# Performance work log

Measured on AMD Instinct MI355X. Metric: run time of the kernel, lower is better.

## Reference

```python
import jax, jax.numpy as jnp
import numpy as np

HEADS = 8
DIM_HEAD = 64
SCALE = DIM_HEAD ** (-0.5)


def _flatten_like_module(t):
    # Reproduces: jnp.transpose(t, (0,2,1,3)).reshape(t.shape[0], t.shape[1], t.shape[2]*t.shape[3])
    # where the reshape dims come from the ORIGINAL (pre-transpose) shape.
    B, S, H, Dh = t.shape
    return jnp.transpose(t, (0, 2, 1, 3)).reshape(B, S, H * Dh)


def _heads_to_batch(t):
    b, s, d = t.shape
    t = t.reshape(b, s, HEADS, d // HEADS)
    t = jnp.transpose(t, (0, 2, 1, 3))
    return t.reshape(b * HEADS, s, d // HEADS)


def setup_inputs() -> dict:
    key = jax.random.key(0)
    kq, kk, kv = jax.random.split(key, 3)
    shape = (2, 16384, 8, 64)  # [B, S, heads, dim_head]
    return {
        "query": jax.random.normal(kq, shape, dtype=jnp.float32),
        "key": jax.random.normal(kk, shape, dtype=jnp.float32),
        "value": jax.random.normal(kv, shape, dtype=jnp.float32),
    }


def reference(query, key, value):
    q = _heads_to_batch(_flatten_like_module(query))   # [B*H, S, Dh]
    k = _heads_to_batch(_flatten_like_module(key))     # [B*H, S, Dh]
    # Swapped contraction: reduce over the sequence axis -> [B*H, Dh, Dh]
    scores = jnp.einsum('bdi,bdj->bij', q, k) * SCALE
    probs = jax.nn.softmax(scores, axis=2)
    v = _heads_to_batch(_flatten_like_module(value))   # [B*H, S, Dh]
    # NOTE: computed in the original module but never returned (dead under jit DCE)
    _hidden = jnp.einsum('bij,bdj->bid', probs, v)     # [B*H, Dh, S]
    return probs
```

## Files before the change

### kernel.cpp

```cpp
#include <hip/hip_runtime.h>

#define NS 16384
#define BUCKETS 16

__device__ __forceinline__ void gload_lds16(const float* g, float* l) {
    __builtin_amdgcn_global_load_lds(
        (const __attribute__((address_space(1))) void*)g,
        (__attribute__((address_space(3))) void*)l,
        16 , 0, 0);
}

__global__ __launch_bounds__(256) void gram_partial(
    const float* __restrict__ Q, const float* __restrict__ K,
    float* __restrict__ part, int bpb, int shi_per_blk)
{
    const int bid    = blockIdx.x;
    const int bucket = bid / bpb;
    const int chunk  = bid % bpb;
    const int b      = bucket >> 3;
    const int r      = bucket & 7;

    const int tid  = threadIdx.x;
    const int lane = tid & 63;
    const int wv   = tid >> 6;
    const int ty   = tid >> 4;
    const int tx   = tid & 15;

    __shared__ __align__(16) float sbuf[2][4096];

    const float* gq = Q + (size_t)b * ((size_t)NS * 512)
                        + ((size_t)wv * 8 + r) * 512 + lane * 4;
    const float* gk = K + (size_t)b * ((size_t)NS * 512)
                        + ((size_t)wv * 8 + r) * 512 + lane * 4;
    const size_t base_off = (size_t)chunk * shi_per_blk * 4096;

    const int niter = shi_per_blk >> 2;

    auto stage = [&](int it, int bufi) {
        const size_t off = base_off + (size_t)it * 16384;
        float* dq = &sbuf[bufi][wv * 512];
        float* dk = &sbuf[bufi][2048 + wv * 512];
        gload_lds16(gq + off, dq);
        gload_lds16(gq + off + 256, dq + 256);
        gload_lds16(gk + off, dk);
        gload_lds16(gk + off + 256, dk + 256);
    };

    float acc[4][4] = {};

    stage(0, 0);
    for (int it = 0; it < niter; ++it) {
        __syncthreads();
        if (it + 1 < niter) stage(it + 1, (it + 1) & 1);
        const float* bq = &sbuf[it & 1][0];
        const float* bk = &sbuf[it & 1][2048];
        #pragma unroll
        for (int tr = 0; tr < 32; ++tr) {
            const float4 qv = *(const float4*)(bq + tr * 64 + ty * 4);
            const float4 kv = *(const float4*)(bk + tr * 64 + tx * 4);
            const float qa[4] = {qv.x, qv.y, qv.z, qv.w};
            const float ka[4] = {kv.x, kv.y, kv.z, kv.w};
            #pragma unroll
            for (int ii = 0; ii < 4; ++ii)
                #pragma unroll
                for (int jj = 0; jj < 4; ++jj)
                    acc[ii][jj] += qa[ii] * ka[jj];
        }
    }

    float* p = part + (size_t)bid * 4096;
    #pragma unroll
    for (int ii = 0; ii < 4; ++ii) {
        float4 v = make_float4(acc[ii][0], acc[ii][1], acc[ii][2], acc[ii][3]);
        *(float4*)(p + (ty * 4 + ii) * 64 + tx * 4) = v;
    }
}

__global__ __launch_bounds__(256) void reduce_softmax(
    const float* __restrict__ part, float* __restrict__ out, int slices)
{
    const int g   = blockIdx.x >> 6;
    const int row = blockIdx.x & 63;
    const int c   = threadIdx.x & 63;
    const int sl  = threadIdx.x >> 6;

    const float* p = part + (size_t)(g * (slices * 4) + sl * slices) * 4096
                          + row * 64 + c;
    float s = 0.f;
    #pragma unroll 4
    for (int k = 0; k < slices; ++k) s += p[(size_t)k * 4096];

    __shared__ float red[4][64];
    red[sl][c] = s;
    __syncthreads();
    if (sl == 0) {
        float v = (red[0][c] + red[1][c]) + (red[2][c] + red[3][c]);
        v *= 0.125f;
        float m = v;
        #pragma unroll
        for (int o = 32; o; o >>= 1) m = fmaxf(m, __shfl_xor(m, o));
        const float e = __expf(v - m);
        float sum = e;
        #pragma unroll
        for (int o = 32; o; o >>= 1) sum += __shfl_xor(sum, o);
        out[(size_t)g * 4096 + row * 64 + c] = e / sum;
    }
}

extern "C" void kernel_launch(void* const* d_in, const int* in_sizes, int n_in,
                              void* d_out, int out_size, void* d_ws, size_t ws_size,
                              hipStream_t stream)
{
    const float* Q = (const float*)d_in[0];
    const float* K = (const float*)d_in[1];
    float* out  = (float*)d_out;
    float* part = (float*)d_ws;

    int bpb = 64;
    while ((size_t)BUCKETS * bpb * 4096 * sizeof(float) > ws_size && bpb > 4) bpb >>= 1;
    const int shi_per_blk = 2048 / bpb;

    gram_partial<<<dim3(BUCKETS * bpb), dim3(256), 0, stream>>>(Q, K, part, bpb, shi_per_blk);
    reduce_softmax<<<dim3(1024), dim3(256), 0, stream>>>(part, out, bpb / 4);
}
```

Before: 189.4 us.

## Replace LDS-staged gram accumulation with direct global loads per wave quadrant

Removes the double-buffered LDS staging (global_load_lds plus __syncthreads) and has each wave compute one 32x32 quadrant of the 64x64 Gram tile, loading float4 values straight from global memory. Launch bounds now request 4 blocks per CU, which should raise occupancy. The aim is to drop LDS traffic and barrier stalls. The cost is redundant global loads, since each Q/K element is now read by two waves and the accesses are strided, so the kernel leans on the L1/L2 caches.

```diff
diff --git a/kernel.cpp b/kernel.cpp
--- a/kernel.cpp
+++ b/kernel.cpp
@@ -3,16 +3,9 @@
 #define NS 16384
 #define BUCKETS 16
 
-__device__ __forceinline__ void gload_lds16(const float* g, float* l) {
-    __builtin_amdgcn_global_load_lds(
-        (const __attribute__((address_space(1))) void*)g,
-        (__attribute__((address_space(3))) void*)l,
-        16 , 0, 0);
-}
-
-__global__ __launch_bounds__(256) void gram_partial(
+__global__ __launch_bounds__(256, 4) void gram_partial(
     const float* __restrict__ Q, const float* __restrict__ K,
-    float* __restrict__ part, int bpb, int shi_per_blk)
+    float* __restrict__ part, int bpb, int spb)
 {
     const int bid    = blockIdx.x;
     const int bucket = bid / bpb;
@@ -20,44 +13,27 @@
     const int b      = bucket >> 3;
     const int r      = bucket & 7;
 
-    const int tid  = threadIdx.x;
-    const int lane = tid & 63;
-    const int wv   = tid >> 6;
-    const int ty   = tid >> 4;
-    const int tx   = tid & 15;
+    const int lane = threadIdx.x & 63;
+    const int wv   = threadIdx.x >> 6;
+    const int ty   = lane >> 3;
+    const int tx   = lane & 7;
+    const int qcol = (wv >> 1) * 32 + ty * 4;
+    const int kcol = (wv & 1) * 32 + tx * 4;
 
-    __shared__ __align__(16) float sbuf[2][4096];
-
-    const float* gq = Q + (size_t)b * ((size_t)NS * 512)
-                        + ((size_t)wv * 8 + r) * 512 + lane * 4;
-    const float* gk = K + (size_t)b * ((size_t)NS * 512)
-                        + ((size_t)wv * 8 + r) * 512 + lane * 4;
-    const size_t base_off = (size_t)chunk * shi_per_blk * 4096;
-
-    const int niter = shi_per_blk >> 2;
-
-    auto stage = [&](int it, int bufi) {
-        const size_t off = base_off + (size_t)it * 16384;
-        float* dq = &sbuf[bufi][wv * 512];
-        float* dk = &sbuf[bufi][2048 + wv * 512];
-        gload_lds16(gq + off, dq);
-        gload_lds16(gq + off + 256, dq + 256);
-        gload_lds16(gk + off, dk);
-        gload_lds16(gk + off + 256, dk + 256);
-    };
+    const size_t tb = (size_t)b * ((size_t)NS * 512) + (size_t)r * 512;
+    const float* qp = Q + tb + qcol;
+    const float* kp = K + tb + kcol;
 
     float acc[4][4] = {};
 
-    stage(0, 0);
-    for (int it = 0; it < niter; ++it) {
-        __syncthreads();
-        if (it + 1 < niter) stage(it + 1, (it + 1) & 1);
-        const float* bq = &sbuf[it & 1][0];
-        const float* bk = &sbuf[it & 1][2048];
+    const int s0 = chunk * spb;
+    for (int s = s0; s < s0 + spb; ++s) {
+        const float* qb = qp + (size_t)s * 4096;
+        const float* kb = kp + (size_t)s * 4096;
         #pragma unroll
-        for (int tr = 0; tr < 32; ++tr) {
-            const float4 qv = *(const float4*)(bq + tr * 64 + ty * 4);
-            const float4 kv = *(const float4*)(bk + tr * 64 + tx * 4);
+        for (int h = 0; h < 8; ++h) {
+            const float4 qv = *(const float4*)(qb + h * 64);
+            const float4 kv = *(const float4*)(kb + h * 64);
             const float qa[4] = {qv.x, qv.y, qv.z, qv.w};
             const float ka[4] = {kv.x, kv.y, kv.z, kv.w};
             #pragma unroll
@@ -68,7 +44,8 @@
         }
     }
 
-    float* p = part + (size_t)bid * 4096;
+    float* p = part + (size_t)bid * 4096
+             + (size_t)((wv >> 1) * 32) * 64 + (wv & 1) * 32;
     #pragma unroll
     for (int ii = 0; ii < 4; ++ii) {
         float4 v = make_float4(acc[ii][0], acc[ii][1], acc[ii][2], acc[ii][3]);
@@ -118,8 +95,8 @@
 
     int bpb = 64;
     while ((size_t)BUCKETS * bpb * 4096 * sizeof(float) > ws_size && bpb > 4) bpb >>= 1;
-    const int shi_per_blk = 2048 / bpb;
+    const int spb = 2048 / bpb;
 
-    gram_partial<<<dim3(BUCKETS * bpb), dim3(256), 0, stream>>>(Q, K, part, bpb, shi_per_blk);
+    gram_partial<<<dim3(BUCKETS * bpb), dim3(256), 0, stream>>>(Q, K, part, bpb, spb);
     reduce_softmax<<<dim3(1024), dim3(256), 0, stream>>>(part, out, bpb / 4);
 }
```

New measurement: 248.1 us. 1.31x slower.
